# Optimization experiments

Measured on AMD Instinct MI355X. Metric: run time of the kernel, lower is better.

## Reference

```python
import jax, jax.numpy as jnp
import numpy as np

D_MODEL = 256
N_HEADS = 8
HEAD_DIM = D_MODEL // N_HEADS


def setup_inputs() -> dict:
    key = jax.random.key(0)
    ks = jax.random.split(key, 10)
    B, L, D = 2, 2048, D_MODEL
    s = 1.0 / np.sqrt(D)
    inp = {
        "x": jax.random.normal(ks[0], (B, L, D), dtype=jnp.float32),
        "Wq": jax.random.normal(ks[1], (D, D), dtype=jnp.float32) * s,
        "bq": jnp.zeros((D,), jnp.float32),
        "Wk": jax.random.normal(ks[2], (D, D), dtype=jnp.float32) * s,
        "bk": jnp.zeros((D,), jnp.float32),
        "Wv": jax.random.normal(ks[3], (D, D), dtype=jnp.float32) * s,
        "bv": jnp.zeros((D,), jnp.float32),
        "u": jax.random.normal(ks[4], (N_HEADS, 1, 1), dtype=jnp.float32) * 0.1,
        "Wo": jax.random.normal(ks[5], (D, D), dtype=jnp.float32) * s,
        "bo": jnp.zeros((D,), jnp.float32),
    }
    return inp


def reference(x, Wq, bq, Wk, bk, Wv, bv, u, Wo, bo):
    B, L, D = x.shape
    H, hd = N_HEADS, HEAD_DIM

    def proj(W, b):  # torch Linear: x @ W.T + b -> [B,H,L,hd]
        return (x @ W.T + b).reshape(B, L, H, hd).transpose(0, 2, 1, 3)

    Q, K, V = proj(Wq, bq), proj(Wk, bk), proj(Wv, bv)

    scores = jnp.einsum("bhqd,bhkd->bhqk", Q, K) / np.sqrt(hd)
    attn_series = jax.nn.softmax(scores, axis=-1)  # [B,H,L,L]

    pos = jnp.arange(L, dtype=jnp.float32)
    dist = jnp.abs(pos[None, :] - pos[:, None])  # [L,L]
    # prior per head: exp(-d^2 / (2*(u^2+1e-6))), normalized over last dim
    prior = jnp.exp(-(dist[None] ** 2) / (2.0 * (u ** 2 + 1e-6)))  # [H,L,L]
    prior = prior / (prior.sum(axis=-1, keepdims=True) + 1e-6)

    discrepancy = jnp.abs(attn_series - prior[None]).mean(axis=(1, 2))  # [B,L]

    out = jnp.einsum("bhqk,bhkd->bhqd", attn_series, V)
    out = out.transpose(0, 2, 1, 3).reshape(B, L, D)
    out = out @ Wo.T + bo
    return out, discrepancy
```

## Files before the change

### kernel.cpp

```cpp
#include <hip/hip_runtime.h>
#include <hip/hip_bf16.h>
#include <math.h>

#define LSEQ 2048
#define DMODEL 256
#define NH 8
#define HD 32

typedef __attribute__((ext_vector_type(8))) short bf16x8;
typedef __attribute__((ext_vector_type(4))) float f32x4;

#define MFMA __builtin_amdgcn_mfma_f32_16x16x32_bf16

__device__ __forceinline__ short f2bf(float x) {
  __hip_bfloat16 h = __float2bfloat16(x);
  return __builtin_bit_cast(short, h);
}
__device__ __forceinline__ float bf2f(short s) {
  __hip_bfloat16 h = __builtin_bit_cast(__hip_bfloat16, s);
  return __bfloat162float(h);
}
__device__ __forceinline__ short bftrunc(float x) {
  return (short)(__builtin_bit_cast(unsigned int, x) >> 16);
}
__device__ __forceinline__ float fexp2(float x) {
#if __has_builtin(__builtin_amdgcn_exp2f)
  return __builtin_amdgcn_exp2f(x);
#else
  return __expf(x * 0.6931471805599453f);
#endif
}
__device__ __forceinline__ unsigned int packtrunc(float lo, float hi) {
  return __builtin_amdgcn_perm(__builtin_bit_cast(unsigned int, hi),
                               __builtin_bit_cast(unsigned int, lo),
                               0x07060302u);
}

__global__ __launch_bounds__(256) void aux_kernel(
    const float* __restrict__ x,
    const float* __restrict__ Wq, const float* __restrict__ Wk,
    const float* __restrict__ Wv, const float* __restrict__ Wo,
    const float* __restrict__ u,
    short* __restrict__ xh,
    short* __restrict__ Wh,
    short* __restrict__ Woh, short* __restrict__ Wol,
    float* __restrict__ Eb, float* __restrict__ Zb)
{
  __shared__ float Cs[LSEQ];
  __shared__ float part[256];
  const int tid = threadIdx.x;
  if (blockIdx.x < 1024) {
    const int i4 = (blockIdx.x * 256 + tid) * 4;
    float4 v = *(const float4*)(x + i4);
    *(short4*)(xh + i4) = make_short4(f2bf(v.x), f2bf(v.y), f2bf(v.z), f2bf(v.w));
    return;
  }
  const int bx = blockIdx.x - 1024;
  if (bx < 256) {
    const int i4 = (bx * 256 + tid) * 4;
    if (i4 < 196608) {
      int row = i4 >> 8, col = i4 & 255;
      const float* W = (row < 256) ? Wq : (row < 512) ? Wk : Wv;
      float4 v = *(const float4*)(W + (row & 255) * 256 + col);
      *(short4*)(Wh + i4) = make_short4(f2bf(v.x), f2bf(v.y), f2bf(v.z), f2bf(v.w));
    } else {
      int j = i4 - 196608;
      float4 v = *(const float4*)(Wo + j);
      short h0 = f2bf(v.x), h1 = f2bf(v.y), h2 = f2bf(v.z), h3 = f2bf(v.w);
      *(short4*)(Woh + j) = make_short4(h0, h1, h2, h3);
      *(short4*)(Wol + j) = make_short4(bftrunc(v.x - bf2f(h0)), bftrunc(v.y - bf2f(h1)),
                                        bftrunc(v.z - bf2f(h2)), bftrunc(v.w - bf2f(h3)));
    }
    return;
  }
  const int h = bx - 256;
  const float uu = u[h];
  const float den = 2.0f * (uu * uu + 1e-6f);
  float e[8]; float run = 0.f;
  const int base = tid * 8;
#pragma unroll
  for (int j = 0; j < 8; ++j) {
    float d = (float)(base + j);
    e[j] = __expf(-(d * d) / den);
    run += e[j];
  }
  part[tid] = run;
  __syncthreads();
  for (int off = 1; off < 256; off <<= 1) {
    float v = (tid >= off) ? part[tid - off] : 0.f;
    __syncthreads();
    part[tid] += v;
    __syncthreads();
  }
  float c = part[tid] - run;
#pragma unroll
  for (int j = 0; j < 8; ++j) {
    c += e[j];
    Cs[base + j] = c;
    Eb[h * LSEQ + base + j] = e[j];
  }
  __syncthreads();
  const float E0 = Cs[0];
  for (int i = tid; i < LSEQ; i += 256) {
    float s = Cs[i] + Cs[LSEQ - 1 - i] - E0;
    Zb[h * LSEQ + i] = 1.0f / (s + 1e-6f);
  }
}

__global__ __launch_bounds__(256) void qkv_gemm(
    const short* __restrict__ xh,
    const short* __restrict__ Bh,
    const float* __restrict__ bq, const float* __restrict__ bk,
    const float* __restrict__ bv,
    short* __restrict__ Qf, short* __restrict__ Kf, short* __restrict__ Vf)
{
  const int tid = threadIdx.x, w = tid >> 6, lane = tid & 63;
  const int l15 = lane & 15, q4 = lane >> 4;
  const int m0 = blockIdx.x * 64, n0 = blockIdx.y * 64;
  const int mrow = m0 + w * 16 + l15;
  f32x4 acc[4] = {{0,0,0,0},{0,0,0,0},{0,0,0,0},{0,0,0,0}};
  for (int k0 = 0; k0 < 256; k0 += 32) {
    bf16x8 ah = *(const bf16x8*)&xh[(size_t)mrow * 256 + k0 + q4 * 8];
#pragma unroll
    for (int nt = 0; nt < 4; ++nt) {
      const size_t bi = (size_t)(n0 + nt * 16 + l15) * 256 + k0 + q4 * 8;
      bf16x8 bh = *(const bf16x8*)&Bh[bi];
      acc[nt] = MFMA(ah, bh, acc[nt], 0, 0, 0);
    }
  }
  const int type = n0 >> 8;
  const int n0l = n0 & 255;
  const float* bias = (type == 0) ? bq : (type == 1) ? bk : bv;
  const float qls = 0.25503489f;
#pragma unroll
  for (int nt = 0; nt < 4; ++nt) {
    const int col = n0l + nt * 16 + l15;
    const float bvv = bias[col];
    const int hh = col >> 5, dloc = col & 31;
#pragma unroll
    for (int r = 0; r < 4; ++r) {
      const int m = m0 + w * 16 + q4 * 4 + r;
      float v = acc[nt][r] + bvv;
      const int bb = m >> 11, mm = m & 2047, rr = mm & 15;
      if (type == 2) {
        const int kt128 = mm >> 7, low7 = mm & 127;
        const int wv = (low7 >> 4) & 3, ph = low7 >> 6;
        const int c = ph * 16 + rr;
        const size_t idx =
          ((((((size_t)bb * 8 + hh) * 16 + kt128) * 4 + wv) * 2 + (dloc >> 4)) * 64
           + (c >> 3) * 16 + (dloc & 15)) * 8 + (c & 7);
        Vf[idx] = f2bf(v);
      } else if (type == 0) {
        const int qblk = mm >> 5, rg = (mm >> 4) & 1;
        const size_t idx =
          (((((size_t)bb * 8 + hh) * 64 + qblk) * 2 + rg) * 64
           + (dloc >> 3) * 16 + rr) * 8 + (dloc & 7);
        Qf[idx] = f2bf(v * qls);
      } else {
        const int g = mm >> 4;
        const size_t idx =
          ((((size_t)bb * 8 + hh) * 128 + g) * 64
           + (dloc >> 3) * 16 + rr) * 8 + (dloc & 7);
        Kf[idx] = f2bf(v);
      }
    }
  }
}

__global__ __launch_bounds__(1024, 8) void attn_kernel(
    const short* __restrict__ Qf, const short* __restrict__ Kf,
    const short* __restrict__ Vf,
    const float* __restrict__ Eb, const float* __restrict__ Zb,
    short* __restrict__ Ohb, short* __restrict__ Olb,
    short* __restrict__ Dp)
{
  __shared__ short Pt[16][16][36];
  __shared__ float Elds[192];
  __shared__ float lpart[16][16];
  __shared__ float lpn[16];
  __shared__ float liz[16];

  const int tid = threadIdx.x, w = tid >> 6, lane = tid & 63;
  const int l15 = lane & 15, q4 = lane >> 4;
  const int flat = blockIdx.x + 128 * (blockIdx.y + 8 * blockIdx.z);
  const int slot = flat >> 3;
  const int g = (flat & 7) | ((slot >> 7) << 3);
  const int h = g & 7, b = g >> 3;
  const int qslot = slot & 127, q0 = qslot * 16;
  const int bh = b * NH + h;

  if (tid < 192) Elds[tid] = Eb[h * LSEQ + tid];
  if (tid < 16)  liz[tid] = Zb[h * LSEQ + q0 + tid];

  const bf16x8* Qf8 = (const bf16x8*)Qf;
  const bf16x8* Kf8 = (const bf16x8*)Kf;
  const bf16x8* Vf8 = (const bf16x8*)Vf;

  bf16x8 qh = Qf8[((size_t)bh * 128 + qslot) * 64 + lane];

  const size_t kfb = (size_t)bh * 128;
  const size_t vfb = (size_t)bh * 16;
  const int wv = w & 3, wq = w >> 2;

  unsigned int pc[4][4];
  float lac[4] = {0.f, 0.f, 0.f, 0.f};
  f32x4 oacc[2] = {{0,0,0,0},{0,0,0,0}};

#pragma unroll
  for (int it = 0; it < 4; ++it) {
    const int kt128 = wq + 4 * it;
    const int gk = kt128 * 8 + wv;
    bf16x8 k0 = Kf8[(kfb + gk) * 64 + lane];
    bf16x8 k1 = Kf8[(kfb + gk + 4) * 64 + lane];
    bf16x8 vb0 = Vf8[(((vfb + kt128) * 4 + wv) * 2 + 0) * 64 + lane];
    bf16x8 vb1 = Vf8[(((vfb + kt128) * 4 + wv) * 2 + 1) * 64 + lane];
    f32x4 s0 = {0.f,0.f,0.f,0.f}; s0 = MFMA(qh, k0, s0, 0, 0, 0);
    f32x4 s1 = {0.f,0.f,0.f,0.f}; s1 = MFMA(qh, k1, s1, 0, 0, 0);
    float p0[4], p1[4];
#pragma unroll
    for (int r = 0; r < 4; ++r) {
      p0[r] = fexp2(s0[r]);
      p1[r] = fexp2(s1[r]);
      lac[r] += p0[r] + p1[r];
      Pt[w][q4 * 4 + r][l15]      = bftrunc(p0[r]);
      Pt[w][q4 * 4 + r][16 + l15] = bftrunc(p1[r]);
    }
    pc[it][0] = packtrunc(p0[0], p0[1]);
    pc[it][1] = packtrunc(p0[2], p0[3]);
    pc[it][2] = packtrunc(p1[0], p1[1]);
    pc[it][3] = packtrunc(p1[2], p1[3]);
    bf16x8 pa = *(const bf16x8*)&Pt[w][l15][q4 * 8];
    oacc[0] = MFMA(pa, vb0, oacc[0], 0, 0, 0);
    oacc[1] = MFMA(pa, vb1, oacc[1], 0, 0, 0);
  }

#pragma unroll
  for (int r = 0; r < 4; ++r) {
    float v = lac[r];
    v += __shfl_xor(v, 1); v += __shfl_xor(v, 2);
    v += __shfl_xor(v, 4); v += __shfl_xor(v, 8);
    if (l15 == 0) lpart[w][q4 * 4 + r] = v;
  }
  __syncthreads();
  if (tid < 16) {
    float l = 0.f;
#pragma unroll
    for (int w16 = 0; w16 < 16; ++w16) l += lpart[w16][tid];
    lpn[tid] = 1.0f / l;
  }
  __syncthreads();

  float pn4[4], iz4[4];
#pragma unroll
  for (int r = 0; r < 4; ++r) {
    pn4[r] = lpn[q4 * 4 + r];
    iz4[r] = liz[q4 * 4 + r];
  }
  const int qrow0 = q0 + q4 * 4;

  const size_t drow = (size_t)(g * 128 + qslot) * LSEQ;
#pragma unroll
  for (int it = 0; it < 4; ++it) {
    const int kt128 = wq + 4 * it;
#pragma unroll
    for (int ph = 0; ph < 2; ++ph) {
      const int c0g = kt128 * 128 + ph * 64 + wv * 16;
      const int kg = c0g + l15;
      const int dd = c0g - q0;
      const bool near = (dd >= -96) && (dd <= 96);
      const unsigned int wlo = pc[it][ph * 2 + 0];
      const unsigned int whi = pc[it][ph * 2 + 1];
      float pr[4];
      pr[0] = __builtin_bit_cast(float, wlo << 16);
      pr[1] = __builtin_bit_cast(float, wlo & 0xffff0000u);
      pr[2] = __builtin_bit_cast(float, whi << 16);
      pr[3] = __builtin_bit_cast(float, whi & 0xffff0000u);
      float dsum = 0.f;
      if (near) {
#pragma unroll
        for (int r = 0; r < 4; ++r) {
          float p = pr[r] * pn4[r];
          int qrow = qrow0 + r;
          int dist = (qrow >= kg) ? (qrow - kg) : (kg - qrow);
          dsum += fabsf(p - Elds[dist] * iz4[r]);
        }
      } else {
        dsum = pr[0] * pn4[0] + pr[1] * pn4[1] + pr[2] * pn4[2] + pr[3] * pn4[3];
      }
      dsum += __shfl_xor(dsum, 16);
      dsum += __shfl_xor(dsum, 32);
      if (q4 == 0) Dp[drow + kg] = f2bf(dsum);
    }
  }

  __syncthreads();
  float* Ored = (float*)Pt;
#pragma unroll
  for (int dt = 0; dt < 2; ++dt) {
#pragma unroll
    for (int r = 0; r < 4; ++r)
      Ored[(w * 16 + q4 * 4 + r) * 17 + l15] = oacc[dt][r];
    __syncthreads();
    if (tid < 256) {
      const int q = tid >> 4, d = tid & 15;
      float v = 0.f;
#pragma unroll
      for (int w16 = 0; w16 < 16; ++w16) v += Ored[(w16 * 16 + q) * 17 + d];
      v *= lpn[q];
      const size_t oo = ((size_t)b * LSEQ + q0 + q) * DMODEL + h * HD + dt * 16 + d;
      short hi = f2bf(v);
      Ohb[oo] = hi;
      Olb[oo] = bftrunc(v - bf2f(hi));
    }
    __syncthreads();
  }
}

__global__ __launch_bounds__(256) void tail_kernel(
    const short* __restrict__ Ah, const short* __restrict__ Al,
    const short* __restrict__ Bh, const short* __restrict__ Bl,
    const float* __restrict__ bias, float* __restrict__ C,
    const short* __restrict__ Dp, float* __restrict__ disc)
{
  __shared__ float red[8][33];
  const int tid = threadIdx.x;
  if (blockIdx.x < 512) {
    const int w = tid >> 6, lane = tid & 63;
    const int l15 = lane & 15, q4 = lane >> 4;
    const int m0 = (blockIdx.x & 63) * 64, n0 = (blockIdx.x >> 6) * 32;
    const int mrow = m0 + w * 16 + l15;
    f32x4 acc[2] = {{0,0,0,0},{0,0,0,0}};
    for (int k0 = 0; k0 < 256; k0 += 32) {
      bf16x8 ah = *(const bf16x8*)&Ah[(size_t)mrow * 256 + k0 + q4 * 8];
      bf16x8 al = *(const bf16x8*)&Al[(size_t)mrow * 256 + k0 + q4 * 8];
#pragma unroll
      for (int nt = 0; nt < 2; ++nt) {
        const size_t bi = (size_t)(n0 + nt * 16 + l15) * 256 + k0 + q4 * 8;
        bf16x8 bh = *(const bf16x8*)&Bh[bi];
        bf16x8 bl = *(const bf16x8*)&Bl[bi];
        acc[nt] = MFMA(ah, bh, acc[nt], 0, 0, 0);
        acc[nt] = MFMA(al, bh, acc[nt], 0, 0, 0);
        acc[nt] = MFMA(ah, bl, acc[nt], 0, 0, 0);
      }
    }
#pragma unroll
    for (int nt = 0; nt < 2; ++nt) {
      const int col = n0 + nt * 16 + l15;
      const float bvv = bias[col];
#pragma unroll
      for (int r = 0; r < 4; ++r) {
        const int m = m0 + w * 16 + q4 * 4 + r;
        C[(size_t)m * 256 + col] = acc[nt][r] + bvv;
      }
    }
    return;
  }
  const int bid = blockIdx.x - 512;
  const int b = bid >> 6, kb = (bid & 63) * 32;
  const int k = kb + (tid & 31), sg = tid >> 5;
  float acc = 0.f;
  const short* base = Dp + ((size_t)b * 1024 + (size_t)sg * 128) * LSEQ + k;
#pragma unroll 4
  for (int i = 0; i < 128; ++i) acc += bf2f(base[(size_t)i * LSEQ]);
  red[sg][tid & 31] = acc;
  __syncthreads();
  if (tid < 32) {
    float v = 0.f;
#pragma unroll
    for (int s2 = 0; s2 < 8; ++s2) v += red[s2][tid];
    disc[b * LSEQ + kb + tid] = v * (1.0f / ((float)NH * (float)LSEQ));
  }
}

extern "C" void kernel_launch(void* const* d_in, const int* in_sizes, int n_in,
                              void* d_out, int out_size, void* d_ws, size_t ws_size,
                              hipStream_t stream)
{
  const float* x  = (const float*)d_in[0];
  const float* Wq = (const float*)d_in[1];
  const float* bq = (const float*)d_in[2];
  const float* Wk = (const float*)d_in[3];
  const float* bk = (const float*)d_in[4];
  const float* Wv = (const float*)d_in[5];
  const float* bv = (const float*)d_in[6];
  const float* u  = (const float*)d_in[7];
  const float* Wo = (const float*)d_in[8];
  const float* bo = (const float*)d_in[9];

  float* out  = (float*)d_out;
  float* disc = out + (size_t)2 * LSEQ * DMODEL;

  char* w8 = (char*)d_ws;
  const size_t MB = 1u << 20;
  short* Qfb = (short*)(w8);
  short* Kfb = (short*)(w8 + 2 * MB);
  short* Vfb = (short*)(w8 + 4 * MB);
  short* Ohb = (short*)(w8 + 6 * MB);
  short* Olb = (short*)(w8 + 8 * MB);
  short* Wh  = (short*)(w8 + 10 * MB);
  short* Woh = (short*)(w8 + 10 * MB + 393216);
  short* Wol = (short*)(w8 + 10 * MB + 524288);
  float* Eb  = (float*)(w8 + 11 * MB);
  float* Zb  = (float*)(w8 + 11 * MB + 65536);
  short* xh  = (short*)(w8 + 12 * MB);
  short* Dp  = (short*)(w8 + 14 * MB);

  aux_kernel<<<1288, 256, 0, stream>>>(x, Wq, Wk, Wv, Wo, u, xh, Wh, Woh, Wol, Eb, Zb);
  qkv_gemm<<<dim3(64, 12), 256, 0, stream>>>(xh, Wh, bq, bk, bv, Qfb, Kfb, Vfb);
  attn_kernel<<<dim3(128, 8, 2), 1024, 0, stream>>>(Qfb, Kfb, Vfb, Eb, Zb,
                                                    Ohb, Olb, Dp);
  tail_kernel<<<640, 256, 0, stream>>>(Ohb, Olb, Woh, Wol, bo, out, Dp, disc);
}
```

Baseline: 157.4 us.

## Store GEMM operands in MFMA fragment-tiled layout for coalesced loads

The x, Wqkv, Wo and attention-output buffers are now written by their producer kernels in a tiled layout matching the 16x16x32 MFMA operand fragment, so each lane loads one contiguous 16-byte chunk. Before, each lane read 16 bytes from a row 512 bytes apart. This targets strided global loads in the QKV and output-projection GEMMs. The cost is more complex index math in the producers and scattered 8-byte stores when converting x and the weights.

New measurement: 142.0 us. 9.8% less time.

```diff
diff --git a/kernel.cpp b/kernel.cpp
--- a/kernel.cpp
+++ b/kernel.cpp
@@ -36,14 +36,15 @@
                                0x07060302u);
 }
 
+
 __global__ __launch_bounds__(256) void aux_kernel(
     const float* __restrict__ x,
     const float* __restrict__ Wq, const float* __restrict__ Wk,
     const float* __restrict__ Wv, const float* __restrict__ Wo,
     const float* __restrict__ u,
-    short* __restrict__ xh,
-    short* __restrict__ Wh,
-    short* __restrict__ Woh, short* __restrict__ Wol,
+    short* __restrict__ xf,
+    short* __restrict__ Wf,
+    short* __restrict__ Wof, short* __restrict__ Wolf,
     float* __restrict__ Eb, float* __restrict__ Zb)
 {
   __shared__ float Cs[LSEQ];
@@ -51,25 +52,36 @@
   const int tid = threadIdx.x;
   if (blockIdx.x < 1024) {
     const int i4 = (blockIdx.x * 256 + tid) * 4;
+    const int row = i4 >> 8, col = i4 & 255;
     float4 v = *(const float4*)(x + i4);
-    *(short4*)(xh + i4) = make_short4(f2bf(v.x), f2bf(v.y), f2bf(v.z), f2bf(v.w));
+    const size_t dst =
+      ((((size_t)(row >> 4) * 8 + (col >> 5)) * 64) + ((col >> 3) & 3) * 16 + (row & 15)) * 8
+      + (col & 7);
+    *(short4*)(xf + dst) = make_short4(f2bf(v.x), f2bf(v.y), f2bf(v.z), f2bf(v.w));
     return;
   }
   const int bx = blockIdx.x - 1024;
   if (bx < 256) {
     const int i4 = (bx * 256 + tid) * 4;
     if (i4 < 196608) {
-      int row = i4 >> 8, col = i4 & 255;
+      const int row = i4 >> 8, col = i4 & 255;
       const float* W = (row < 256) ? Wq : (row < 512) ? Wk : Wv;
       float4 v = *(const float4*)(W + (row & 255) * 256 + col);
-      *(short4*)(Wh + i4) = make_short4(f2bf(v.x), f2bf(v.y), f2bf(v.z), f2bf(v.w));
+      const size_t dst =
+        ((((size_t)(row >> 4) * 8 + (col >> 5)) * 64) + ((col >> 3) & 3) * 16 + (row & 15)) * 8
+        + (col & 7);
+      *(short4*)(Wf + dst) = make_short4(f2bf(v.x), f2bf(v.y), f2bf(v.z), f2bf(v.w));
     } else {
-      int j = i4 - 196608;
+      const int j = i4 - 196608;
+      const int row = j >> 8, col = j & 255;
       float4 v = *(const float4*)(Wo + j);
       short h0 = f2bf(v.x), h1 = f2bf(v.y), h2 = f2bf(v.z), h3 = f2bf(v.w);
-      *(short4*)(Woh + j) = make_short4(h0, h1, h2, h3);
-      *(short4*)(Wol + j) = make_short4(bftrunc(v.x - bf2f(h0)), bftrunc(v.y - bf2f(h1)),
-                                        bftrunc(v.z - bf2f(h2)), bftrunc(v.w - bf2f(h3)));
+      const size_t dst =
+        ((((size_t)(row >> 4) * 8 + (col >> 5)) * 64) + ((col >> 3) & 3) * 16 + (row & 15)) * 8
+        + (col & 7);
+      *(short4*)(Wof + dst) = make_short4(h0, h1, h2, h3);
+      *(short4*)(Wolf + dst) = make_short4(bftrunc(v.x - bf2f(h0)), bftrunc(v.y - bf2f(h1)),
+                                           bftrunc(v.z - bf2f(h2)), bftrunc(v.w - bf2f(h3)));
     }
     return;
   }
@@ -108,8 +120,8 @@
 }
 
 __global__ __launch_bounds__(256) void qkv_gemm(
-    const short* __restrict__ xh,
-    const short* __restrict__ Bh,
+    const short* __restrict__ xf,
+    const short* __restrict__ Wf,
     const float* __restrict__ bq, const float* __restrict__ bk,
     const float* __restrict__ bv,
     short* __restrict__ Qf, short* __restrict__ Kf, short* __restrict__ Vf)
@@ -117,14 +129,15 @@
   const int tid = threadIdx.x, w = tid >> 6, lane = tid & 63;
   const int l15 = lane & 15, q4 = lane >> 4;
   const int m0 = blockIdx.x * 64, n0 = blockIdx.y * 64;
-  const int mrow = m0 + w * 16 + l15;
+  const bf16x8* xf8 = (const bf16x8*)xf;
+  const bf16x8* wf8 = (const bf16x8*)Wf;
+  const int mg8 = ((m0 >> 4) + w) * 8;
   f32x4 acc[4] = {{0,0,0,0},{0,0,0,0},{0,0,0,0},{0,0,0,0}};
-  for (int k0 = 0; k0 < 256; k0 += 32) {
-    bf16x8 ah = *(const bf16x8*)&xh[(size_t)mrow * 256 + k0 + q4 * 8];
+  for (int kc = 0; kc < 8; ++kc) {
+    bf16x8 ah = xf8[(mg8 + kc) * 64 + lane];
 #pragma unroll
     for (int nt = 0; nt < 4; ++nt) {
-      const size_t bi = (size_t)(n0 + nt * 16 + l15) * 256 + k0 + q4 * 8;
-      bf16x8 bh = *(const bf16x8*)&Bh[bi];
+      bf16x8 bh = wf8[(((n0 >> 4) + nt) * 8 + kc) * 64 + lane];
       acc[nt] = MFMA(ah, bh, acc[nt], 0, 0, 0);
     }
   }
@@ -171,7 +184,7 @@
     const short* __restrict__ Qf, const short* __restrict__ Kf,
     const short* __restrict__ Vf,
     const float* __restrict__ Eb, const float* __restrict__ Zb,
-    short* __restrict__ Ohb, short* __restrict__ Olb,
+    short* __restrict__ Ofb, short* __restrict__ Olfb,
     short* __restrict__ Dp)
 {
   __shared__ short Pt[16][16][36];
@@ -295,6 +308,7 @@
 
   __syncthreads();
   float* Ored = (float*)Pt;
+  const size_t obase = ((size_t)(b * 128 + qslot) * 8 + h) * 64;
 #pragma unroll
   for (int dt = 0; dt < 2; ++dt) {
 #pragma unroll
@@ -307,18 +321,18 @@
 #pragma unroll
       for (int w16 = 0; w16 < 16; ++w16) v += Ored[(w16 * 16 + q) * 17 + d];
       v *= lpn[q];
-      const size_t oo = ((size_t)b * LSEQ + q0 + q) * DMODEL + h * HD + dt * 16 + d;
+      const size_t oo = (obase + ((dt * 16 + d) >> 3) * 16 + q) * 8 + (d & 7);
       short hi = f2bf(v);
-      Ohb[oo] = hi;
-      Olb[oo] = bftrunc(v - bf2f(hi));
+      Ofb[oo] = hi;
+      Olfb[oo] = bftrunc(v - bf2f(hi));
     }
     __syncthreads();
   }
 }
 
 __global__ __launch_bounds__(256) void tail_kernel(
-    const short* __restrict__ Ah, const short* __restrict__ Al,
-    const short* __restrict__ Bh, const short* __restrict__ Bl,
+    const short* __restrict__ Ofb, const short* __restrict__ Olfb,
+    const short* __restrict__ Wof, const short* __restrict__ Wolf,
     const float* __restrict__ bias, float* __restrict__ C,
     const short* __restrict__ Dp, float* __restrict__ disc)
 {
@@ -328,16 +342,19 @@
     const int w = tid >> 6, lane = tid & 63;
     const int l15 = lane & 15, q4 = lane >> 4;
     const int m0 = (blockIdx.x & 63) * 64, n0 = (blockIdx.x >> 6) * 32;
-    const int mrow = m0 + w * 16 + l15;
+    const bf16x8* Ah8 = (const bf16x8*)Ofb;
+    const bf16x8* Al8 = (const bf16x8*)Olfb;
+    const bf16x8* Bh8 = (const bf16x8*)Wof;
+    const bf16x8* Bl8 = (const bf16x8*)Wolf;
+    const int mg8 = ((m0 >> 4) + w) * 8;
     f32x4 acc[2] = {{0,0,0,0},{0,0,0,0}};
-    for (int k0 = 0; k0 < 256; k0 += 32) {
-      bf16x8 ah = *(const bf16x8*)&Ah[(size_t)mrow * 256 + k0 + q4 * 8];
-      bf16x8 al = *(const bf16x8*)&Al[(size_t)mrow * 256 + k0 + q4 * 8];
+    for (int kc = 0; kc < 8; ++kc) {
+      bf16x8 ah = Ah8[(mg8 + kc) * 64 + lane];
+      bf16x8 al = Al8[(mg8 + kc) * 64 + lane];
 #pragma unroll
       for (int nt = 0; nt < 2; ++nt) {
-        const size_t bi = (size_t)(n0 + nt * 16 + l15) * 256 + k0 + q4 * 8;
-        bf16x8 bh = *(const bf16x8*)&Bh[bi];
-        bf16x8 bl = *(const bf16x8*)&Bl[bi];
+        bf16x8 bh = Bh8[(((n0 >> 4) + nt) * 8 + kc) * 64 + lane];
+        bf16x8 bl = Bl8[(((n0 >> 4) + nt) * 8 + kc) * 64 + lane];
         acc[nt] = MFMA(ah, bh, acc[nt], 0, 0, 0);
         acc[nt] = MFMA(al, bh, acc[nt], 0, 0, 0);
         acc[nt] = MFMA(ah, bl, acc[nt], 0, 0, 0);
@@ -392,22 +409,22 @@
 
   char* w8 = (char*)d_ws;
   const size_t MB = 1u << 20;
-  short* Qfb = (short*)(w8);
-  short* Kfb = (short*)(w8 + 2 * MB);
-  short* Vfb = (short*)(w8 + 4 * MB);
-  short* Ohb = (short*)(w8 + 6 * MB);
-  short* Olb = (short*)(w8 + 8 * MB);
-  short* Wh  = (short*)(w8 + 10 * MB);
-  short* Woh = (short*)(w8 + 10 * MB + 393216);
-  short* Wol = (short*)(w8 + 10 * MB + 524288);
-  float* Eb  = (float*)(w8 + 11 * MB);
-  float* Zb  = (float*)(w8 + 11 * MB + 65536);
-  short* xh  = (short*)(w8 + 12 * MB);
-  short* Dp  = (short*)(w8 + 14 * MB);
-
-  aux_kernel<<<1288, 256, 0, stream>>>(x, Wq, Wk, Wv, Wo, u, xh, Wh, Woh, Wol, Eb, Zb);
-  qkv_gemm<<<dim3(64, 12), 256, 0, stream>>>(xh, Wh, bq, bk, bv, Qfb, Kfb, Vfb);
+  short* Qfb  = (short*)(w8);
+  short* Kfb  = (short*)(w8 + 2 * MB);
+  short* Vfb  = (short*)(w8 + 4 * MB);
+  short* Ofb  = (short*)(w8 + 6 * MB);
+  short* Olfb = (short*)(w8 + 8 * MB);
+  short* Wf   = (short*)(w8 + 10 * MB);
+  short* Wof  = (short*)(w8 + 10 * MB + 393216);
+  short* Wolf = (short*)(w8 + 10 * MB + 524288);
+  float* Eb   = (float*)(w8 + 11 * MB);
+  float* Zb   = (float*)(w8 + 11 * MB + 65536);
+  short* xf   = (short*)(w8 + 12 * MB);
+  short* Dp   = (short*)(w8 + 14 * MB);
+
+  aux_kernel<<<1288, 256, 0, stream>>>(x, Wq, Wk, Wv, Wo, u, xf, Wf, Wof, Wolf, Eb, Zb);
+  qkv_gemm<<<dim3(64, 12), 256, 0, stream>>>(xf, Wf, bq, bk, bv, Qfb, Kfb, Vfb);
   attn_kernel<<<dim3(128, 8, 2), 1024, 0, stream>>>(Qfb, Kfb, Vfb, Eb, Zb,
-                                                    Ohb, Olb, Dp);
-  tail_kernel<<<640, 256, 0, stream>>>(Ohb, Olb, Woh, Wol, bo, out, Dp, disc);
-}
+                                                    Ofb, Olfb, Dp);
+  tail_kernel<<<640, 256, 0, stream>>>(Ofb, Olfb, Wof, Wolf, bo, out, Dp, disc);
+}
```
